# Kernel optimization log

Hardware: AMD Instinct MI355X
Metric: run time of the kernel (lower is better)

Reference implementation:

```python
import jax, jax.numpy as jnp
import numpy as np

EPS = 1e-5

def layernorm(x, g, b):
    mu = jnp.mean(x, axis=-1, keepdims=True)
    var = jnp.mean((x - mu) ** 2, axis=-1, keepdims=True)
    return (x - mu) * jax.lax.rsqrt(var + EPS) * g + b

def cswin_attn(q, k, v, lepe_w, lepe_b, H, W, H_sp, W_sp, num_heads):
    # q,k,v: (B, L, C) with C = branch dim
    B, L, C = q.shape
    d = C // num_heads
    nH, nW = H // H_sp, W // W_sp
    def to_win(t):
        t = t.transpose(0, 2, 1).reshape(B, C, nH, H_sp, nW, W_sp)
        t = t.transpose(0, 2, 4, 3, 5, 1).reshape(B * nH * nW, H_sp * W_sp, num_heads, d)
        return t.transpose(0, 2, 1, 3)  # (Bw, h, N, d)
    kw = to_win(k)
    vw = to_win(v)
    # q windows as images for LePE depthwise conv
    qi = q.transpose(0, 2, 1).reshape(B, C, nH, H_sp, nW, W_sp)
    qi = qi.transpose(0, 2, 4, 1, 3, 5).reshape(B * nH * nW, C, H_sp, W_sp)
    lepe = jax.lax.conv_general_dilated(qi, lepe_w, (1, 1), 'SAME',
                                        feature_group_count=C,
                                        dimension_numbers=('NCHW', 'OIHW', 'NCHW'))
    lepe = lepe + lepe_b[None, :, None, None]
    lepe = lepe.reshape(-1, num_heads, d, H_sp * W_sp).transpose(0, 1, 3, 2)
    qw = qi.reshape(-1, num_heads, d, H_sp * W_sp).transpose(0, 1, 3, 2) * (float(d) ** -0.5)
    attn = jax.nn.softmax(jnp.einsum('whnd,whmd->whnm', qw, kw), axis=-1)
    out = jnp.einsum('whnm,whmd->whnd', attn, vw) + lepe  # (Bw, h, N, d)
    out = out.transpose(0, 2, 1, 3).reshape(B, nH, nW, H_sp, W_sp, C)
    out = out.transpose(0, 1, 3, 2, 4, 5).reshape(B, H * W, C)
    return out

def setup_inputs() -> dict:
    key = jax.random.key(0)
    ks = jax.random.split(key, 20)
    B, C, H, W = 8, 128, 64, 64
    ch_z = 512
    hid = 4 * C
    Cb = C // 2  # branch dim
    s = lambda fin: (1.0 / np.sqrt(fin))
    inp = {
        'x': jax.random.normal(ks[0], (B, C, H, W), jnp.float32),
        'z': jax.random.normal(ks[1], (B, ch_z), jnp.float32),
        'ln1_g': jnp.ones((C,), jnp.float32), 'ln1_b': jnp.zeros((C,), jnp.float32),
        'ln2_g': jnp.ones((C,), jnp.float32), 'ln2_b': jnp.zeros((C,), jnp.float32),
        'Wz1': jax.random.normal(ks[2], (C, ch_z), jnp.float32) * s(ch_z),
        'Wz2': jax.random.normal(ks[3], (C, ch_z), jnp.float32) * s(ch_z),
        'Wqkv': jax.random.normal(ks[4], (3 * C, C), jnp.float32) * s(C),
        'Wproj': jax.random.normal(ks[5], (C, C), jnp.float32) * s(C),
        'bproj': jnp.zeros((C,), jnp.float32),
        'lepe_w0': jax.random.normal(ks[6], (Cb, 1, 3, 3), jnp.float32) * (1.0 / 3.0),
        'lepe_b0': jnp.zeros((Cb,), jnp.float32),
        'lepe_w1': jax.random.normal(ks[7], (Cb, 1, 3, 3), jnp.float32) * (1.0 / 3.0),
        'lepe_b1': jnp.zeros((Cb,), jnp.float32),
        'W1': jax.random.normal(ks[8], (hid, C), jnp.float32) * s(C),
        'b1': jnp.zeros((hid,), jnp.float32),
        'W2': jax.random.normal(ks[9], (C, hid), jnp.float32) * s(hid),
        'b2': jnp.zeros((C,), jnp.float32),
    }
    return inp

def reference(x, z, ln1_g, ln1_b, ln2_g, ln2_b, Wz1, Wz2, Wqkv, Wproj, bproj,
              lepe_w0, lepe_b0, lepe_w1, lepe_b1, W1, b1, W2, b2):
    B, C, H, W = x.shape
    nh = 4  # num_heads // 2 per branch
    ss = 8  # split_size
    Cb = C // 2
    xf = x.reshape(B, C, H * W).transpose(0, 2, 1)  # (B, L, C)
    # code-conditioned attention branch
    z1 = z @ Wz1.T  # (B, C)
    h1 = layernorm(xf, ln1_g, ln1_b) + z1[:, None, :]
    qkv = (h1 @ Wqkv.T).reshape(B, H * W, 3, C).transpose(2, 0, 1, 3)  # (3, B, L, C)
    q, k, v = qkv[0], qkv[1], qkv[2]
    x1 = cswin_attn(q[..., :Cb], k[..., :Cb], v[..., :Cb], lepe_w0, lepe_b0, H, W, H, ss, nh)
    x2 = cswin_attn(q[..., Cb:], k[..., Cb:], v[..., Cb:], lepe_w1, lepe_b1, H, W, ss, W, nh)
    att = jnp.concatenate([x1, x2], axis=2) @ Wproj.T + bproj
    xf = xf + att
    # code-conditioned MLP branch
    z2 = z @ Wz2.T
    h2 = layernorm(xf, ln2_g, ln2_b) + z2[:, None, :]
    mlp = jax.nn.gelu(h2 @ W1.T + b1, approximate=False) @ W2.T + b2
    xf = xf + mlp
    return xf.transpose(0, 2, 1).reshape(B, C, H, W)
```

## Files before the change

### kernel.cpp

```cpp
#include <hip/hip_runtime.h>
#include <cstddef>

__device__ __forceinline__ float b2f(unsigned short u) {
  return __uint_as_float(((unsigned int)u) << 16);
}
__device__ __forceinline__ unsigned short f2b(float f) {
  unsigned int u = __float_as_uint(f);
  u = u + 0x7FFFu + ((u >> 16) & 1u);
  return (unsigned short)(u >> 16);
}
__device__ __forceinline__ unsigned int cvtpk(float lo, float hi) {
  unsigned int r;
  asm("v_cvt_pk_bf16_f32 %0, %1, %2" : "=v"(r) : "v"(lo), "v"(hi));
  return r;
}
__device__ __forceinline__ float gelu_exact(float x) {
  return 0.5f * x * (1.0f + erff(x * 0.70710678118654752f));
}

#if defined(__has_builtin)
#if __has_builtin(__builtin_amdgcn_exp2f)
#define EXP2(x) __builtin_amdgcn_exp2f(x)
#else
#define EXP2(x) __expf((x) * 0.6931471805599453f)
#endif
#else
#define EXP2(x) __expf((x) * 0.6931471805599453f)
#endif

typedef __attribute__((ext_vector_type(8))) short bf16x8;
typedef __attribute__((ext_vector_type(4))) float f32x4;

__device__ __forceinline__ unsigned int dtype_flag(const unsigned short* gref) {
  return (gref[0] == 0x3F80u) ? 1u : 0u;
}

struct Ptrs18 { const void* p[18]; };
__constant__ const int c_off[19] = {
    0, 4096, 4224, 4352, 4480, 4608, 70144, 135680, 184832, 201216,
    201344, 201920, 201984, 202560, 202624, 268160, 268672, 334208, 334336};

__global__ __launch_bounds__(256) void k_convert(Ptrs18 ptrs,
                                                 unsigned short* __restrict__ dst) {
  int idx = blockIdx.x * 256 + threadIdx.x;
  if (idx >= 334336) return;
  unsigned int flag = dtype_flag((const unsigned short*)ptrs.p[1]);
  int i = 0;
#pragma unroll
  for (int t = 1; t < 18; ++t) i += (idx >= c_off[t]);
  int local = idx - c_off[i];
  if (flag) dst[idx] = ((const unsigned short*)ptrs.p[i])[local];
  else      dst[idx] = f2b(((const float*)ptrs.p[i])[local]);
}

__global__ __launch_bounds__(256) void k_transpose_in(const void* __restrict__ x,
                                                      const unsigned short* __restrict__ gref,
                                                      float* __restrict__ xf) {
  __shared__ float t[32][33];
  unsigned int flag = dtype_flag(gref);
  int b = blockIdx.z;
  int l0 = blockIdx.x * 32, c0 = blockIdx.y * 32;
  int tx = threadIdx.x & 31, ty = threadIdx.x >> 5;
#pragma unroll
  for (int i = 0; i < 32; i += 8) {
    size_t gi = ((size_t)b * 128 + c0 + ty + i) * 4096 + l0 + tx;
    t[ty + i][tx] = flag ? b2f(((const unsigned short*)x)[gi]) : ((const float*)x)[gi];
  }
  __syncthreads();
#pragma unroll
  for (int i = 0; i < 32; i += 8)
    xf[((size_t)b * 4096 + l0 + ty + i) * 128 + c0 + tx] = t[tx][ty + i];
}

__global__ __launch_bounds__(256) void k_zmm(const unsigned short* __restrict__ z,
                                             const unsigned short* __restrict__ Wz1,
                                             const unsigned short* __restrict__ Wz2,
                                             float* __restrict__ zz) {
  __shared__ float sz[512];
  int b = blockIdx.x, tid = threadIdx.x;
  sz[tid]       = b2f(z[b * 512 + tid]);
  sz[tid + 256] = b2f(z[b * 512 + 256 + tid]);
  __syncthreads();
  const unsigned short* W = (tid < 128) ? Wz1 : Wz2;
  int c = tid & 127;
  const unsigned short* wr = W + c * 512;
  float acc = 0.f;
  for (int k = 0; k < 512; k += 4) {
    ushort4 wv = *(const ushort4*)&wr[k];
    acc += b2f(wv.x) * sz[k] + b2f(wv.y) * sz[k + 1] + b2f(wv.z) * sz[k + 2] + b2f(wv.w) * sz[k + 3];
  }
  zz[b * 256 + tid] = acc;
}

__global__ __launch_bounds__(256) void k_ln(const float* __restrict__ x,
                                            const unsigned short* __restrict__ g,
                                            const unsigned short* __restrict__ bb,
                                            const float* __restrict__ zz, int zsel,
                                            unsigned short* __restrict__ out) {
  int row = blockIdx.x * 4 + (threadIdx.x >> 6);
  int lane = threadIdx.x & 63;
  int b = row >> 12;
  const float* xr = x + (size_t)row * 128;
  float2 v = *(const float2*)&xr[lane * 2];
  float s = v.x + v.y, s2 = v.x * v.x + v.y * v.y;
#pragma unroll
  for (int m = 32; m; m >>= 1) {
    s += __shfl_xor(s, m, 64);
    s2 += __shfl_xor(s2, m, 64);
  }
  float mu = s * 0.0078125f;
  float var = s2 * 0.0078125f - mu * mu;
  float rstd = rsqrtf(var + 1e-5f);
  int c = lane * 2;
  const float* zr = zz + b * 256 + zsel * 128;
  float ox = (v.x - mu) * rstd * b2f(g[c])     + b2f(bb[c])     + zr[c];
  float oy = (v.y - mu) * rstd * b2f(g[c + 1]) + b2f(bb[c + 1]) + zr[c + 1];
  ushort2 o2; o2.x = f2b(ox); o2.y = f2b(oy);
  *(ushort2*)&out[(size_t)row * 128 + c] = o2;
}

__global__ __launch_bounds__(256) void k_gemm_mfma(const unsigned short* __restrict__ A,
                                                   const unsigned short* __restrict__ W,
                                                   const unsigned short* __restrict__ bias,
                                                   const float* __restrict__ res,
                                                   void* __restrict__ out,
                                                   int M, int N, int K, int ldw, int flags) {
  __shared__ unsigned short As[128][136];
  int bm = blockIdx.x * 128, bn = blockIdx.y * 128;
  int tid = threadIdx.x;
  int lane = tid & 63, wv = tid >> 6;
  int wm = (wv >> 1) * 64, wn = (wv & 1) * 64;
  int qd = lane >> 4, l15 = lane & 15;
#pragma unroll
  for (int i = tid; i < 2048; i += 256) {
    int row = i >> 4, c8 = (i & 15) << 3;
    *(bf16x8*)&As[row][c8] = *(const bf16x8*)&A[(size_t)(bm + row) * 128 + c8];
  }
  __syncthreads();
  f32x4 acc[4][4] = {};
#pragma unroll
  for (int ks = 0; ks < 4; ++ks) {
    bf16x8 af[4], bfr[4];
#pragma unroll
    for (int t = 0; t < 4; ++t) {
      af[t]  = *(const bf16x8*)&As[wm + t * 16 + l15][ks * 32 + qd * 8];
      bfr[t] = *(const bf16x8*)&W[(size_t)(bn + wn + t * 16 + l15) * ldw + ks * 32 + qd * 8];
    }
#pragma unroll
    for (int mi = 0; mi < 4; ++mi)
#pragma unroll
      for (int nj = 0; nj < 4; ++nj)
        acc[mi][nj] = __builtin_amdgcn_mfma_f32_16x16x32_bf16(af[mi], bfr[nj],
                                                              acc[mi][nj], 0, 0, 0);
  }
  if (flags & 4) {
#pragma unroll
    for (int mi = 0; mi < 4; ++mi)
#pragma unroll
      for (int r = 0; r < 4; ++r) {
        int row = bm + wm + mi * 16 + qd * 4 + r;
        int bb2 = row >> 12, l = row & 4095;
        int hI = l >> 6, wI = l & 63;
        int s0 = wI >> 3, t0 = hI * 8 + (wI & 7);
        int s1 = hI >> 3, t1 = (hI & 7) * 64 + wI;
#pragma unroll
        for (int nj = 0; nj < 4; ++nj) {
          int colb = bn + wn + nj * 16;
          int kv = colb >> 7, br = (colb >> 6) & 1, hh2 = (colb >> 4) & 3;
          int ss = br ? s1 : s0, tt = br ? t1 : t0;
          size_t addr = ((((size_t)((kv * 8 + bb2) * 2 + br) * 4 + hh2) * 8 + ss) * 512 + tt) * 16 + l15;
          ((unsigned short*)out)[addr] = f2b(acc[mi][nj][r]);
        }
      }
    return;
  }
  float bv[4];
#pragma unroll
  for (int nj = 0; nj < 4; ++nj)
    bv[nj] = bias ? b2f(bias[bn + wn + nj * 16 + l15]) : 0.f;
#pragma unroll
  for (int mi = 0; mi < 4; ++mi) {
#pragma unroll
    for (int r = 0; r < 4; ++r) {
      int row = bm + wm + mi * 16 + qd * 4 + r;
#pragma unroll
      for (int nj = 0; nj < 4; ++nj) {
        int col = bn + wn + nj * 16 + l15;
        float t = acc[mi][nj][r] + bv[nj];
        if (res) t += res[(size_t)row * N + col];
        if (flags & 2) ((unsigned short*)out)[(size_t)row * N + col] = f2b(t);
        else           ((float*)out)[(size_t)row * N + col] = t;
      }
    }
  }
}

__global__ __launch_bounds__(256, 4) void k_gemm32(const unsigned short* __restrict__ A,
                                                   const unsigned short* __restrict__ W,
                                                   const unsigned short* __restrict__ bias,
                                                   const float* __restrict__ res,
                                                   void* __restrict__ out,
                                                   int M, int N, int K, int ldw, int flags) {
  __shared__ unsigned short As[32][136];
  int bm = blockIdx.x * 32, bn = blockIdx.y * 128;
  int tid = threadIdx.x;
  int lane = tid & 63, wv = tid >> 6;
  int qd = lane >> 4, l15 = lane & 15;
  {
    int i = tid;
    int row = i >> 4, c8 = (i & 15) << 3;
    *(bf16x8*)&As[row][c8] = *(const bf16x8*)&A[(size_t)(bm + row) * 128 + c8];
    i += 256; row = i >> 4; c8 = (i & 15) << 3;
    *(bf16x8*)&As[row][c8] = *(const bf16x8*)&A[(size_t)(bm + row) * 128 + c8];
  }
  __syncthreads();
  f32x4 acc[2][2] = {};
#pragma unroll
  for (int ks = 0; ks < 4; ++ks) {
    bf16x8 af[2], bfr[2];
#pragma unroll
    for (int t = 0; t < 2; ++t)
      af[t] = *(const bf16x8*)&As[t * 16 + l15][ks * 32 + qd * 8];
#pragma unroll
    for (int t = 0; t < 2; ++t)
      bfr[t] = *(const bf16x8*)&W[(size_t)(bn + wv * 32 + t * 16 + l15) * ldw + ks * 32 + qd * 8];
#pragma unroll
    for (int mi = 0; mi < 2; ++mi)
#pragma unroll
      for (int nj = 0; nj < 2; ++nj)
        acc[mi][nj] = __builtin_amdgcn_mfma_f32_16x16x32_bf16(af[mi], bfr[nj],
                                                              acc[mi][nj], 0, 0, 0);
  }
  float bv[2];
#pragma unroll
  for (int nj = 0; nj < 2; ++nj)
    bv[nj] = bias ? b2f(bias[bn + wv * 32 + nj * 16 + l15]) : 0.f;
#pragma unroll
  for (int mi = 0; mi < 2; ++mi) {
#pragma unroll
    for (int r = 0; r < 4; ++r) {
      int row = bm + mi * 16 + qd * 4 + r;
#pragma unroll
      for (int nj = 0; nj < 2; ++nj) {
        int col = bn + wv * 32 + nj * 16 + l15;
        float t = acc[mi][nj][r] + bv[nj];
        if (flags & 1) t = gelu_exact(t);
        if (res) t += res[(size_t)row * N + col];
        if (flags & 2) ((unsigned short*)out)[(size_t)row * N + col] = f2b(t);
        else           ((float*)out)[(size_t)row * N + col] = t;
      }
    }
  }
}

__global__ __launch_bounds__(256, 4) void k_mlp(const float* __restrict__ xf,
                                                const unsigned short* __restrict__ g,
                                                const unsigned short* __restrict__ bb,
                                                const float* __restrict__ zz,
                                                const unsigned short* __restrict__ W1,
                                                const unsigned short* __restrict__ b1,
                                                const unsigned short* __restrict__ W2,
                                                const unsigned short* __restrict__ b2,
                                                const unsigned short* __restrict__ gref,
                                                void* __restrict__ outp) {
  __shared__ __align__(16) char smem[18944];
  unsigned short (*As_all)[136] = (unsigned short(*)[136])smem;
  unsigned short (*Hs)[32][40]  = (unsigned short(*)[32][40])(smem + 8704);
  int tid = threadIdx.x;
  int bm = blockIdx.x * 32;
  int bidx = bm >> 12;
  {
    int row = tid >> 3, part = tid & 7;
    const float* xr = xf + ((size_t)(bm + row) * 128 + part * 16);
    float v[16];
#pragma unroll
    for (int i = 0; i < 4; ++i) *(float4*)&v[i * 4] = *(const float4*)&xr[i * 4];
    float s = 0.f, s2 = 0.f;
#pragma unroll
    for (int i = 0; i < 16; ++i) { s += v[i]; s2 += v[i] * v[i]; }
    s  += __shfl_xor(s, 1, 64);  s  += __shfl_xor(s, 2, 64);  s  += __shfl_xor(s, 4, 64);
    s2 += __shfl_xor(s2, 1, 64); s2 += __shfl_xor(s2, 2, 64); s2 += __shfl_xor(s2, 4, 64);
    float mu = s * 0.0078125f;
    float var = s2 * 0.0078125f - mu * mu;
    float rstd = rsqrtf(var + 1e-5f);
    const float* zr = zz + bidx * 256 + 128 + part * 16;
#pragma unroll
    for (int i = 0; i < 16; i += 2) {
      int c = part * 16 + i;
      float ox = (v[i]     - mu) * rstd * b2f(g[c])     + b2f(bb[c])     + zr[i];
      float oy = (v[i + 1] - mu) * rstd * b2f(g[c + 1]) + b2f(bb[c + 1]) + zr[i + 1];
      unsigned int u = (unsigned int)f2b(ox) | ((unsigned int)f2b(oy) << 16);
      *(unsigned int*)&As_all[row][c] = u;
    }
  }
  __syncthreads();
  int lane = tid & 63, wv = tid >> 6;
  int qd = lane >> 4, l15 = lane & 15;
  f32x4 acc2[2][2] = {};
#pragma unroll 1
  for (int j = 0; j < 4; ++j) {
    f32x4 acc1[2][2] = {};
    const unsigned short* W1j = W1 + j * 128 * 128;
#pragma unroll
    for (int ks = 0; ks < 4; ++ks) {
      bf16x8 af[2], bfr[2];
#pragma unroll
      for (int t = 0; t < 2; ++t)
        af[t] = *(const bf16x8*)&As_all[t * 16 + l15][ks * 32 + qd * 8];
#pragma unroll
      for (int t = 0; t < 2; ++t)
        bfr[t] = *(const bf16x8*)&W1j[(wv * 32 + t * 16 + l15) * 128 + ks * 32 + qd * 8];
#pragma unroll
      for (int mi = 0; mi < 2; ++mi)
#pragma unroll
        for (int nj = 0; nj < 2; ++nj)
          acc1[mi][nj] = __builtin_amdgcn_mfma_f32_16x16x32_bf16(af[mi], bfr[nj],
                                                                 acc1[mi][nj], 0, 0, 0);
    }
    if (j) __syncthreads();
    float bv1[2];
#pragma unroll
    for (int nj = 0; nj < 2; ++nj)
      bv1[nj] = b2f(b1[j * 128 + wv * 32 + nj * 16 + l15]);
#pragma unroll
    for (int mi = 0; mi < 2; ++mi)
#pragma unroll
      for (int nj = 0; nj < 2; ++nj)
#pragma unroll
        for (int r = 0; r < 4; ++r) {
          float t = gelu_exact(acc1[mi][nj][r] + bv1[nj]);
          Hs[wv][mi * 16 + qd * 4 + r][nj * 16 + l15] = f2b(t);
        }
    __syncthreads();
#pragma unroll
    for (int ks = 0; ks < 4; ++ks) {
      bf16x8 af2[2], bfr2[2];
#pragma unroll
      for (int t = 0; t < 2; ++t)
        af2[t] = *(const bf16x8*)&Hs[ks][t * 16 + l15][qd * 8];
#pragma unroll
      for (int t = 0; t < 2; ++t)
        bfr2[t] = *(const bf16x8*)&W2[(wv * 32 + t * 16 + l15) * 512 + j * 128 + ks * 32 + qd * 8];
#pragma unroll
      for (int mi = 0; mi < 2; ++mi)
#pragma unroll
        for (int nj = 0; nj < 2; ++nj)
          acc2[mi][nj] = __builtin_amdgcn_mfma_f32_16x16x32_bf16(af2[mi], bfr2[nj],
                                                                 acc2[mi][nj], 0, 0, 0);
    }
  }
  float bv2[2];
#pragma unroll
  for (int nj = 0; nj < 2; ++nj)
    bv2[nj] = b2f(b2[wv * 32 + nj * 16 + l15]);
  __syncthreads();
  float* tile = (float*)smem;
#pragma unroll
  for (int mi = 0; mi < 2; ++mi)
#pragma unroll
    for (int r = 0; r < 4; ++r) {
      int row = mi * 16 + qd * 4 + r;
#pragma unroll
      for (int nj = 0; nj < 2; ++nj) {
        int col = wv * 32 + nj * 16 + l15;
        size_t gi = (size_t)(bm + row) * 128 + col;
        tile[col * 36 + row] = acc2[mi][nj][r] + bv2[nj] + xf[gi];
      }
    }
  __syncthreads();
  unsigned int flag = dtype_flag(gref);
  int c = tid >> 1, hf = tid & 1;
  int b = bm >> 12, l0 = (bm & 4095) + hf * 16;
  const float* tr = &tile[c * 36 + hf * 16];
  if (flag) {
    unsigned short* op = (unsigned short*)outp + ((size_t)(b * 128 + c)) * 4096 + l0;
#pragma unroll
    for (int i = 0; i < 16; i += 4) {
      ushort4 o;
      o.x = f2b(tr[i]); o.y = f2b(tr[i + 1]); o.z = f2b(tr[i + 2]); o.w = f2b(tr[i + 3]);
      *(ushort4*)&op[i] = o;
    }
  } else {
    float* op = (float*)outp + ((size_t)(b * 128 + c)) * 4096 + l0;
#pragma unroll
    for (int i = 0; i < 16; i += 4)
      *(float4*)&op[i] = *(const float4*)&tr[i];
  }
}

__global__ __launch_bounds__(256, 4) void k_attn_mfma(const unsigned short* __restrict__ qkvw,
                                                      const unsigned short* __restrict__ lw0,
                                                      const unsigned short* __restrict__ lb0,
                                                      const unsigned short* __restrict__ lw1,
                                                      const unsigned short* __restrict__ lb1,
                                                      unsigned short* __restrict__ att) {
  __shared__ unsigned short Ks[512][16];
  __shared__ unsigned short Vt[16][520];
  const size_t S1 = 4194304;
  int branch = blockIdx.y;
  int bx = blockIdx.x;
  int half = bx & 1, wh = bx >> 1;
  int w = wh >> 2, hh = wh & 3;
  int b = w >> 3, s = w & 7;
  int cb = branch * 64 + hh * 16;
  size_t slab = ((size_t)(((b * 2 + branch) * 4 + hh) * 8 + s)) * 8192;
  const unsigned short* Qg = qkvw + slab;
  const unsigned short* Kg = qkvw + S1 + slab;
  const unsigned short* Vg = qkvw + 2 * S1 + slab;
  int tid = threadIdx.x;
  for (int i = tid; i < 1024; i += 256) {
    int tok = i >> 1, c8 = (i & 1) << 3;
    *(bf16x8*)&Ks[tok][c8] = *(const bf16x8*)&Kg[tok * 16 + c8];
    bf16x8 vv = *(const bf16x8*)&Vg[tok * 16 + c8];
    int col = (tok & ~31) | ((tok & 12) << 1) | ((tok & 16) >> 2) | (tok & 3);
#pragma unroll
    for (int j = 0; j < 8; ++j) Vt[c8 + j][col] = (unsigned short)vv[j];
  }
  __syncthreads();
  int lane = tid & 63, wv = tid >> 6;
  int qd = lane >> 4, l15 = lane & 15;
  int koff = (qd & 1) * 8;
  const unsigned short* lwp = branch ? lw1 : lw0;
  const unsigned short* lbp = branch ? lb1 : lb0;
  float wreg[4][9], breg[4];
#pragma unroll
  for (int r = 0; r < 4; ++r) {
    int cc = hh * 16 + qd * 4 + r;
    breg[r] = b2f(lbp[cc]);
#pragma unroll
    for (int j = 0; j < 9; ++j) wreg[r][j] = b2f(lwp[cc * 9 + j]);
  }
  bf16x8 onesv;
#pragma unroll
  for (int j = 0; j < 8; ++j) onesv[j] = (short)0x3F80;
  int sy = branch ? 64 : 8;
  int yl = branch ? 8 : 64;
  int xl = branch ? 64 : 8;
  const float QSCALE = 0.25f * 1.44269504f;
  const float NS = -11.5415603f;
  const f32x4 NSHIFT = {NS, NS, NS, NS};
#pragma unroll 1
  for (int qt = 0; qt < 4; ++qt) {
    int q0 = half * 256 + wv * 64 + qt * 16;
    int tq = q0 + l15;
    bf16x8 qf = {};
    if (qd < 2) {
      bf16x8 raw = *(const bf16x8*)&Qg[tq * 16 + qd * 8];
#pragma unroll
      for (int j = 0; j < 8; ++j)
        qf[j] = (short)f2b(b2f((unsigned short)raw[j]) * QSCALE);
    }
    f32x4 O0 = {0.f, 0.f, 0.f, 0.f}, O1 = {0.f, 0.f, 0.f, 0.f};
    f32x4 Osum = {0.f, 0.f, 0.f, 0.f};
#pragma unroll 1
    for (int kc = 0; kc < 4; ++kc) {
      f32x4 sc[8];
#pragma unroll
      for (int c = 0; c < 8; ++c) {
        bf16x8 kf = *(const bf16x8*)&Ks[kc * 128 + c * 16 + l15][koff];
        sc[c] = __builtin_amdgcn_mfma_f32_16x16x32_bf16(kf, qf, NSHIFT, 0, 0, 0);
      }
#pragma unroll
      for (int c = 0; c < 8; ++c) {
        float e0 = EXP2(sc[c][0]), e1 = EXP2(sc[c][1]);
        float e2 = EXP2(sc[c][2]), e3 = EXP2(sc[c][3]);
        sc[c][0] = __uint_as_float(cvtpk(e0, e1));
        sc[c][1] = __uint_as_float(cvtpk(e2, e3));
      }
#pragma unroll
      for (int bc = 0; bc < 4; ++bc) {
        union { unsigned int u[4]; bf16x8 v; } pu;
        pu.u[0] = __float_as_uint(sc[2 * bc][0]);
        pu.u[1] = __float_as_uint(sc[2 * bc][1]);
        pu.u[2] = __float_as_uint(sc[2 * bc + 1][0]);
        pu.u[3] = __float_as_uint(sc[2 * bc + 1][1]);
        bf16x8 vf = *(const bf16x8*)&Vt[l15][kc * 128 + bc * 32 + qd * 8];
        Osum = __builtin_amdgcn_mfma_f32_16x16x32_bf16(onesv, pu.v, Osum, 0, 0, 0);
        if (bc & 1) O1 = __builtin_amdgcn_mfma_f32_16x16x32_bf16(vf, pu.v, O1, 0, 0, 0);
        else        O0 = __builtin_amdgcn_mfma_f32_16x16x32_bf16(vf, pu.v, O0, 0, 0, 0);
      }
    }
    int y = branch ? (tq >> 6) : (tq >> 3);
    int x = branch ? (tq & 63) : (tq & 7);
    float lep[4] = {breg[0], breg[1], breg[2], breg[3]};
#pragma unroll
    for (int dy = -1; dy <= 1; ++dy)
#pragma unroll
      for (int dx = -1; dx <= 1; ++dx) {
        if ((unsigned)(y + dy) < (unsigned)yl && (unsigned)(x + dx) < (unsigned)xl) {
          int tn = tq + dy * sy + dx;
          int j = (dy + 1) * 3 + (dx + 1);
          ushort4 qv = *(const ushort4*)&Qg[tn * 16 + qd * 4];
          lep[0] += wreg[0][j] * b2f(qv.x);
          lep[1] += wreg[1][j] * b2f(qv.y);
          lep[2] += wreg[2][j] * b2f(qv.z);
          lep[3] += wreg[3][j] * b2f(qv.w);
        }
      }
    float inv = 1.f / Osum[0];
    int lo = branch ? (s * 8 + y) * 64 + x : y * 64 + s * 8 + x;
    unsigned short* op = att + ((size_t)(b * 4096 + lo)) * 128 + cb + qd * 4;
    ushort4 o;
    o.x = f2b((O0[0] + O1[0]) * inv + lep[0]);
    o.y = f2b((O0[1] + O1[1]) * inv + lep[1]);
    o.z = f2b((O0[2] + O1[2]) * inv + lep[2]);
    o.w = f2b((O0[3] + O1[3]) * inv + lep[3]);
    *(ushort4*)op = o;
  }
}

extern "C" void kernel_launch(void* const* d_in, const int* in_sizes, int n_in,
                              void* d_out, int out_size, void* d_ws, size_t ws_size,
                              hipStream_t stream) {
  const size_t S = 4194304;
  float* ws = (float*)d_ws;
  float* zz = ws + 64;
  unsigned short* norm = (unsigned short*)(ws + 2112);
  float* xf = ws + 169472;
  unsigned short* h   = (unsigned short*)(ws + 169472 + S);
  unsigned short* qkv = (unsigned short*)(ws + 169472 + S + S / 2);
  unsigned short* att = h;

  const unsigned short* z     = norm + 0;
  const unsigned short* ln1g  = norm + 4096;
  const unsigned short* ln1b  = norm + 4224;
  const unsigned short* ln2g  = norm + 4352;
  const unsigned short* ln2b  = norm + 4480;
  const unsigned short* Wz1   = norm + 4608;
  const unsigned short* Wz2   = norm + 70144;
  const unsigned short* Wqkv  = norm + 135680;
  const unsigned short* Wproj = norm + 184832;
  const unsigned short* bproj = norm + 201216;
  const unsigned short* lw0   = norm + 201344;
  const unsigned short* lb0   = norm + 201920;
  const unsigned short* lw1   = norm + 201984;
  const unsigned short* lb1   = norm + 202560;
  const unsigned short* W1    = norm + 202624;
  const unsigned short* b1    = norm + 268160;
  const unsigned short* W2    = norm + 268672;
  const unsigned short* b2    = norm + 334208;

  const unsigned short* gref = (const unsigned short*)d_in[2];

  Ptrs18 ptrs;
  for (int i = 0; i < 18; ++i) ptrs.p[i] = d_in[i + 1];

  dim3 t256(256);
  k_convert<<<dim3(1306), t256, 0, stream>>>(ptrs, (unsigned short*)norm);
  k_transpose_in<<<dim3(128, 4, 8), t256, 0, stream>>>(d_in[0], gref, xf);
  k_zmm<<<dim3(8), t256, 0, stream>>>(z, Wz1, Wz2, zz);
  k_ln<<<dim3(8192), t256, 0, stream>>>(xf, ln1g, ln1b, zz, 0, h);
  k_gemm_mfma<<<dim3(256, 3), t256, 0, stream>>>(h, Wqkv, nullptr, nullptr, qkv,
                                                 32768, 384, 128, 128, 2 | 4);
  k_attn_mfma<<<dim3(512, 2), t256, 0, stream>>>(qkv, lw0, lb0, lw1, lb1, att);
  k_gemm32<<<dim3(1024, 1), t256, 0, stream>>>(att, Wproj, bproj, xf, xf,
                                               32768, 128, 128, 128, 0);
  k_mlp<<<dim3(1024), t256, 0, stream>>>(xf, ln2g, ln2b, zz, W1, b1, W2, b2,
                                         gref, d_out);
}
```

Measured before the change: 224.4 us.

## Prefetch MLP weight fragments into registers and double-buffer hidden tile

```diff
diff --git a/kernel.cpp b/kernel.cpp
--- a/kernel.cpp
+++ b/kernel.cpp
@@ -263,9 +263,9 @@
                                                 const unsigned short* __restrict__ b2,
                                                 const unsigned short* __restrict__ gref,
                                                 void* __restrict__ outp) {
-  __shared__ __align__(16) char smem[18944];
+  __shared__ __align__(16) char smem[29184];
   unsigned short (*As_all)[136] = (unsigned short(*)[136])smem;
-  unsigned short (*Hs)[32][40]  = (unsigned short(*)[32][40])(smem + 8704);
+  unsigned short (*Hs)[4][32][40] = (unsigned short(*)[4][32][40])(smem + 8704);
   int tid = threadIdx.x;
   int bm = blockIdx.x * 32;
   int bidx = bm >> 12;
@@ -296,28 +296,44 @@
   __syncthreads();
   int lane = tid & 63, wv = tid >> 6;
   int qd = lane >> 4, l15 = lane & 15;
+  int wr0 = wv * 32 + l15;
   f32x4 acc2[2][2] = {};
+  bf16x8 w1f[8];
+#pragma unroll
+  for (int ks = 0; ks < 4; ++ks)
+#pragma unroll
+    for (int t = 0; t < 2; ++t)
+      w1f[ks * 2 + t] = *(const bf16x8*)&W1[(wr0 + t * 16) * 128 + ks * 32 + qd * 8];
 #pragma unroll 1
   for (int j = 0; j < 4; ++j) {
+    bf16x8 w2f[8];
+#pragma unroll
+    for (int ks = 0; ks < 4; ++ks)
+#pragma unroll
+      for (int t = 0; t < 2; ++t)
+        w2f[ks * 2 + t] = *(const bf16x8*)&W2[(wr0 + t * 16) * 512 + j * 128 + ks * 32 + qd * 8];
     f32x4 acc1[2][2] = {};
-    const unsigned short* W1j = W1 + j * 128 * 128;
 #pragma unroll
     for (int ks = 0; ks < 4; ++ks) {
-      bf16x8 af[2], bfr[2];
+      bf16x8 af[2];
 #pragma unroll
       for (int t = 0; t < 2; ++t)
         af[t] = *(const bf16x8*)&As_all[t * 16 + l15][ks * 32 + qd * 8];
 #pragma unroll
-      for (int t = 0; t < 2; ++t)
-        bfr[t] = *(const bf16x8*)&W1j[(wv * 32 + t * 16 + l15) * 128 + ks * 32 + qd * 8];
-#pragma unroll
       for (int mi = 0; mi < 2; ++mi)
 #pragma unroll
         for (int nj = 0; nj < 2; ++nj)
-          acc1[mi][nj] = __builtin_amdgcn_mfma_f32_16x16x32_bf16(af[mi], bfr[nj],
+          acc1[mi][nj] = __builtin_amdgcn_mfma_f32_16x16x32_bf16(af[mi], w1f[ks * 2 + nj],
                                                                  acc1[mi][nj], 0, 0, 0);
     }
-    if (j) __syncthreads();
+    if (j < 3) {
+      const unsigned short* W1n = W1 + (j + 1) * 16384;
+#pragma unroll
+      for (int ks = 0; ks < 4; ++ks)
+#pragma unroll
+        for (int t = 0; t < 2; ++t)
+          w1f[ks * 2 + t] = *(const bf16x8*)&W1n[(wr0 + t * 16) * 128 + ks * 32 + qd * 8];
+    }
     float bv1[2];
 #pragma unroll
     for (int nj = 0; nj < 2; ++nj)
@@ -329,23 +345,20 @@
 #pragma unroll
         for (int r = 0; r < 4; ++r) {
           float t = gelu_exact(acc1[mi][nj][r] + bv1[nj]);
-          Hs[wv][mi * 16 + qd * 4 + r][nj * 16 + l15] = f2b(t);
+          Hs[j & 1][wv][mi * 16 + qd * 4 + r][nj * 16 + l15] = f2b(t);
         }
     __syncthreads();
 #pragma unroll
     for (int ks = 0; ks < 4; ++ks) {
-      bf16x8 af2[2], bfr2[2];
+      bf16x8 af2[2];
 #pragma unroll
       for (int t = 0; t < 2; ++t)
-        af2[t] = *(const bf16x8*)&Hs[ks][t * 16 + l15][qd * 8];
-#pragma unroll
-      for (int t = 0; t < 2; ++t)
-        bfr2[t] = *(const bf16x8*)&W2[(wv * 32 + t * 16 + l15) * 512 + j * 128 + ks * 32 + qd * 8];
+        af2[t] = *(const bf16x8*)&Hs[j & 1][ks][t * 16 + l15][qd * 8];
 #pragma unroll
       for (int mi = 0; mi < 2; ++mi)
 #pragma unroll
         for (int nj = 0; nj < 2; ++nj)
-          acc2[mi][nj] = __builtin_amdgcn_mfma_f32_16x16x32_bf16(af2[mi], bfr2[nj],
+          acc2[mi][nj] = __builtin_amdgcn_mfma_f32_16x16x32_bf16(af2[mi], w2f[ks * 2 + nj],
                                                                  acc2[mi][nj], 0, 0, 0);
     }
   }
```

New measurement: 231.7 us. +3.3%, slower.

## Fuse output projection and residual into the MLP kernel via shared-memory tile

Applied to the files above, without the earlier changes.

```diff
diff --git a/kernel.cpp b/kernel.cpp
--- a/kernel.cpp
+++ b/kernel.cpp
@@ -195,86 +195,76 @@
   }
 }
 
-__global__ __launch_bounds__(256, 4) void k_gemm32(const unsigned short* __restrict__ A,
-                                                   const unsigned short* __restrict__ W,
-                                                   const unsigned short* __restrict__ bias,
-                                                   const float* __restrict__ res,
-                                                   void* __restrict__ out,
-                                                   int M, int N, int K, int ldw, int flags) {
-  __shared__ unsigned short As[32][136];
-  int bm = blockIdx.x * 32, bn = blockIdx.y * 128;
+__global__ __launch_bounds__(256, 4) void k_pm(const unsigned short* __restrict__ att,
+                                               const unsigned short* __restrict__ Wp,
+                                               const unsigned short* __restrict__ bp,
+                                               const float* __restrict__ xf,
+                                               const unsigned short* __restrict__ g,
+                                               const unsigned short* __restrict__ bb,
+                                               const float* __restrict__ zz,
+                                               const unsigned short* __restrict__ W1,
+                                               const unsigned short* __restrict__ b1,
+                                               const unsigned short* __restrict__ W2,
+                                               const unsigned short* __restrict__ b2,
+                                               const unsigned short* __restrict__ gref,
+                                               void* __restrict__ outp) {
+  __shared__ __align__(16) char smem[35840];
+  float (*xt)[132] = (float(*)[132])smem;
+  unsigned short (*As_all)[136] = (unsigned short(*)[136])(smem + 16896);
+  unsigned short (*Hs)[32][40]  = (unsigned short(*)[32][40])(smem + 25600);
   int tid = threadIdx.x;
+  int bm = blockIdx.x * 32;
+  int bidx = bm >> 12;
   int lane = tid & 63, wv = tid >> 6;
   int qd = lane >> 4, l15 = lane & 15;
   {
     int i = tid;
     int row = i >> 4, c8 = (i & 15) << 3;
-    *(bf16x8*)&As[row][c8] = *(const bf16x8*)&A[(size_t)(bm + row) * 128 + c8];
+    *(bf16x8*)&As_all[row][c8] = *(const bf16x8*)&att[(size_t)(bm + row) * 128 + c8];
     i += 256; row = i >> 4; c8 = (i & 15) << 3;
-    *(bf16x8*)&As[row][c8] = *(const bf16x8*)&A[(size_t)(bm + row) * 128 + c8];
-  }
-  __syncthreads();
-  f32x4 acc[2][2] = {};
-#pragma unroll
-  for (int ks = 0; ks < 4; ++ks) {
-    bf16x8 af[2], bfr[2];
-#pragma unroll
-    for (int t = 0; t < 2; ++t)
-      af[t] = *(const bf16x8*)&As[t * 16 + l15][ks * 32 + qd * 8];
-#pragma unroll
-    for (int t = 0; t < 2; ++t)
-      bfr[t] = *(const bf16x8*)&W[(size_t)(bn + wv * 32 + t * 16 + l15) * ldw + ks * 32 + qd * 8];
+    *(bf16x8*)&As_all[row][c8] = *(const bf16x8*)&att[(size_t)(bm + row) * 128 + c8];
+  }
+  __syncthreads();
+  {
+    f32x4 acc[2][2] = {};
+#pragma unroll
+    for (int ks = 0; ks < 4; ++ks) {
+      bf16x8 af[2], bfr[2];
+#pragma unroll
+      for (int t = 0; t < 2; ++t)
+        af[t] = *(const bf16x8*)&As_all[t * 16 + l15][ks * 32 + qd * 8];
+#pragma unroll
+      for (int t = 0; t < 2; ++t)
+        bfr[t] = *(const bf16x8*)&Wp[(wv * 32 + t * 16 + l15) * 128 + ks * 32 + qd * 8];
+#pragma unroll
+      for (int mi = 0; mi < 2; ++mi)
+#pragma unroll
+        for (int nj = 0; nj < 2; ++nj)
+          acc[mi][nj] = __builtin_amdgcn_mfma_f32_16x16x32_bf16(af[mi], bfr[nj],
+                                                                acc[mi][nj], 0, 0, 0);
+    }
+    float bv[2];
+#pragma unroll
+    for (int nj = 0; nj < 2; ++nj)
+      bv[nj] = b2f(bp[wv * 32 + nj * 16 + l15]);
 #pragma unroll
     for (int mi = 0; mi < 2; ++mi)
 #pragma unroll
-      for (int nj = 0; nj < 2; ++nj)
-        acc[mi][nj] = __builtin_amdgcn_mfma_f32_16x16x32_bf16(af[mi], bfr[nj],
-                                                              acc[mi][nj], 0, 0, 0);
-  }
-  float bv[2];
-#pragma unroll
-  for (int nj = 0; nj < 2; ++nj)
-    bv[nj] = bias ? b2f(bias[bn + wv * 32 + nj * 16 + l15]) : 0.f;
-#pragma unroll
-  for (int mi = 0; mi < 2; ++mi) {
-#pragma unroll
-    for (int r = 0; r < 4; ++r) {
-      int row = bm + mi * 16 + qd * 4 + r;
-#pragma unroll
-      for (int nj = 0; nj < 2; ++nj) {
-        int col = bn + wv * 32 + nj * 16 + l15;
-        float t = acc[mi][nj][r] + bv[nj];
-        if (flags & 1) t = gelu_exact(t);
-        if (res) t += res[(size_t)row * N + col];
-        if (flags & 2) ((unsigned short*)out)[(size_t)row * N + col] = f2b(t);
-        else           ((float*)out)[(size_t)row * N + col] = t;
-      }
-    }
-  }
-}
-
-__global__ __launch_bounds__(256, 4) void k_mlp(const float* __restrict__ xf,
-                                                const unsigned short* __restrict__ g,
-                                                const unsigned short* __restrict__ bb,
-                                                const float* __restrict__ zz,
-                                                const unsigned short* __restrict__ W1,
-                                                const unsigned short* __restrict__ b1,
-                                                const unsigned short* __restrict__ W2,
-                                                const unsigned short* __restrict__ b2,
-                                                const unsigned short* __restrict__ gref,
-                                                void* __restrict__ outp) {
-  __shared__ __align__(16) char smem[18944];
-  unsigned short (*As_all)[136] = (unsigned short(*)[136])smem;
-  unsigned short (*Hs)[32][40]  = (unsigned short(*)[32][40])(smem + 8704);
-  int tid = threadIdx.x;
-  int bm = blockIdx.x * 32;
-  int bidx = bm >> 12;
+      for (int r = 0; r < 4; ++r) {
+        int row = mi * 16 + qd * 4 + r;
+#pragma unroll
+        for (int nj = 0; nj < 2; ++nj) {
+          int col = wv * 32 + nj * 16 + l15;
+          xt[row][col] = acc[mi][nj][r] + bv[nj] + xf[(size_t)(bm + row) * 128 + col];
+        }
+      }
+  }
+  __syncthreads();
   {
     int row = tid >> 3, part = tid & 7;
-    const float* xr = xf + ((size_t)(bm + row) * 128 + part * 16);
     float v[16];
 #pragma unroll
-    for (int i = 0; i < 4; ++i) *(float4*)&v[i * 4] = *(const float4*)&xr[i * 4];
+    for (int i = 0; i < 4; ++i) *(float4*)&v[i * 4] = *(const float4*)&xt[row][part * 16 + i * 4];
     float s = 0.f, s2 = 0.f;
 #pragma unroll
     for (int i = 0; i < 16; ++i) { s += v[i]; s2 += v[i] * v[i]; }
@@ -294,8 +284,6 @@
     }
   }
   __syncthreads();
-  int lane = tid & 63, wv = tid >> 6;
-  int qd = lane >> 4, l15 = lane & 15;
   f32x4 acc2[2][2] = {};
 #pragma unroll 1
   for (int j = 0; j < 4; ++j) {
@@ -354,7 +342,7 @@
   for (int nj = 0; nj < 2; ++nj)
     bv2[nj] = b2f(b2[wv * 32 + nj * 16 + l15]);
   __syncthreads();
-  float* tile = (float*)smem;
+  float* tile = (float*)(smem + 16896);
 #pragma unroll
   for (int mi = 0; mi < 2; ++mi)
 #pragma unroll
@@ -363,8 +351,7 @@
 #pragma unroll
       for (int nj = 0; nj < 2; ++nj) {
         int col = wv * 32 + nj * 16 + l15;
-        size_t gi = (size_t)(bm + row) * 128 + col;
-        tile[col * 36 + row] = acc2[mi][nj][r] + bv2[nj] + xf[gi];
+        tile[col * 36 + row] = acc2[mi][nj][r] + bv2[nj] + xt[row][col];
       }
     }
   __syncthreads();
@@ -553,8 +540,6 @@
   k_gemm_mfma<<<dim3(256, 3), t256, 0, stream>>>(h, Wqkv, nullptr, nullptr, qkv,
                                                  32768, 384, 128, 128, 2 | 4);
   k_attn_mfma<<<dim3(512, 2), t256, 0, stream>>>(qkv, lw0, lb0, lw1, lb1, att);
-  k_gemm32<<<dim3(1024, 1), t256, 0, stream>>>(att, Wproj, bproj, xf, xf,
-                                               32768, 128, 128, 128, 0);
-  k_mlp<<<dim3(1024), t256, 0, stream>>>(xf, ln2g, ln2b, zz, W1, b1, W2, b2,
-                                         gref, d_out);
-}
+  k_pm<<<dim3(1024), t256, 0, stream>>>(att, Wproj, bproj, xf, ln2g, ln2b, zz,
+                                        W1, b1, W2, b2, gref, d_out);
+}
```

Result: faster. 216.1 us (-3.7%).
